# Kernel optimization log

Measured on AMD Instinct MI355X. Metric: run time of the kernel, lower is better.

Reference implementation:

```python
import jax, jax.numpy as jnp
import numpy as np

K = 1024            # atoms per chain
L = 4 * K - 9       # 2*(K-3) sin/cos dihedrals + (K-2) len13 + (K-1) bond lengths
EPS = 1e-6


def _denorm(v, lo, hi):
    # map [-1, 1] -> [lo, hi]
    return (v + 1.0) * 0.5 * (hi - lo) + lo


def _output_arr2values(v):
    # split flat NN output into (sin/cos dihedrals, hedron len13, bond lengths)
    n_d = K - 3
    sc = v[: 2 * n_d].reshape(n_d, 2)                     # (sin, cos) per dihedral
    d13 = _denorm(v[2 * n_d : 2 * n_d + K - 2], 1.5, 5.0)  # 1-3 distances, [1.5, 5]
    bl = _denorm(v[2 * n_d + K - 2 :], 0.9, 3.0)           # bond lengths,  [0.9, 3]
    return sc, d13, bl


def _len2ang(sc, d13, bl):
    # bond angles via law of cosines from consecutive bond lengths + 1-3 distance
    l1, l2 = bl[:-1], bl[1:]
    ct = (l1 * l1 + l2 * l2 - d13 * d13) / (2.0 * l1 * l2)
    theta = jnp.arccos(jnp.clip(ct, -1.0 + EPS, 1.0 - EPS))   # (K-2,) radians
    chi = jnp.arctan2(sc[:, 0], sc[:, 1])                      # (K-3,) radians
    return theta, chi


def _len_ang2coords(bl, theta, chi):
    # sequential NeRF chain extension: place atom i from atoms i-3, i-2, i-1
    a0 = jnp.zeros(3, dtype=bl.dtype)
    a1 = jnp.array([1.0, 0.0, 0.0], dtype=bl.dtype) * bl[0]
    t0 = theta[0]
    a2 = a1 + bl[1] * jnp.stack([-jnp.cos(t0), jnp.sin(t0), jnp.zeros((), bl.dtype)])

    def step(carry, inp):
        a, b, c = carry
        l, th, ch = inp
        bc = c - b
        bc = bc / (jnp.linalg.norm(bc) + EPS)
        n = jnp.cross(b - a, bc)
        n = n / (jnp.linalg.norm(n) + EPS)
        m = jnp.cross(n, bc)
        st = jnp.sin(th)
        d = c + l * (-jnp.cos(th) * bc + st * jnp.cos(ch) * m + st * jnp.sin(ch) * n)
        return (b, c, d), d

    _, rest = jax.lax.scan(step, (a0, a1, a2), (bl[2:], theta[1:], chi))
    return jnp.concatenate([jnp.stack([a0, a1, a2]), rest], axis=0)  # (K, 3)


def _chain2coords(v):
    sc, d13, bl = _output_arr2values(v)
    theta, chi = _len2ang(sc, d13, bl)
    return _len_ang2coords(bl, theta, chi)


def setup_inputs() -> dict:
    key = jax.random.key(0)
    k1, k2 = jax.random.split(key)
    B = 2048
    predictions = 2.0 * jax.random.uniform(k1, (B, L), dtype=jnp.float32) - 1.0
    targets = 2.0 * jax.random.uniform(k2, (B, L), dtype=jnp.float32) - 1.0
    return {"predictions": predictions, "targets": targets}


def reference(predictions, targets):
    p = jnp.clip(predictions, -1.0, 1.0)           # only predictions are clamped
    pred_coords = jax.vmap(_chain2coords)(p)        # (B, K, 3)
    targ_coords = jax.vmap(_chain2coords)(targets)  # (B, K, 3)
    return jnp.mean(jnp.square(pred_coords - targ_coords))
```

## Files before the change

### kernel.cpp

```cpp
#include <hip/hip_runtime.h>


#define LROW  4087
#define NSTEP 1021
#define NROW  2048
#define CHUNK 8
#define EPSF  1e-6f
#define INVMEAN (1.0f / (2048.0f * 1024.0f * 3.0f))

__device__ __forceinline__ float frcp(float x){ return __builtin_amdgcn_rcpf(x); }
__device__ __forceinline__ float frsq(float x){ return __builtin_amdgcn_rsqf(x); }

struct Xf { float f[12]; };

__device__ __forceinline__ Xf xident(){
  Xf X;
  X.f[0]=1.f; X.f[1]=0.f; X.f[2]=0.f;
  X.f[3]=0.f; X.f[4]=1.f; X.f[5]=0.f;
  X.f[6]=0.f; X.f[7]=0.f; X.f[8]=1.f;
  X.f[9]=0.f; X.f[10]=0.f; X.f[11]=0.f;
  return X;
}

__device__ __forceinline__ Xf xcombine(const Xf& A, const Xf& B){
  Xf C;
  #pragma unroll
  for (int c3 = 0; c3 < 12; c3 += 3){
    const float bx = B.f[c3], by = B.f[c3+1], bz = B.f[c3+2];
    C.f[c3]   = A.f[0]*bx + A.f[3]*by + A.f[6]*bz;
    C.f[c3+1] = A.f[1]*bx + A.f[4]*by + A.f[7]*bz;
    C.f[c3+2] = A.f[2]*bx + A.f[5]*by + A.f[8]*bz;
  }
  C.f[9] += A.f[9]; C.f[10] += A.f[10]; C.f[11] += A.f[11];
  return C;
}

__device__ __forceinline__ void xstepP(Xf& X, float Px, float Py, float Pz){
  const float l2 = Px*Px + Py*Py + Pz*Pz;
  const float q  = frsq(l2);
  const float hx = q*Px, hy = q*Py, hz = q*Pz;
  const float ist = frsq(fmaxf(hy*hy + hz*hz, 1e-12f));
  const float ux = X.f[0]*Px + X.f[3]*Py + X.f[6]*Pz;
  const float uy = X.f[1]*Px + X.f[4]*Py + X.f[7]*Pz;
  const float uz = X.f[2]*Px + X.f[5]*Py + X.f[8]*Pz;
  X.f[9] += ux; X.f[10] += uy; X.f[11] += uz;
  const float n0x = q*ux, n0y = q*uy, n0z = q*uz;
  const float n1x = ist*(hx*n0x - X.f[0]);
  const float n1y = ist*(hx*n0y - X.f[1]);
  const float n1z = ist*(hx*n0z - X.f[2]);
  const float n2x = ist*(hy*X.f[6] - hz*X.f[3]);
  const float n2y = ist*(hy*X.f[7] - hz*X.f[4]);
  const float n2z = ist*(hy*X.f[8] - hz*X.f[5]);
  X.f[0]=n0x; X.f[1]=n0y; X.f[2]=n0z;
  X.f[3]=n1x; X.f[4]=n1y; X.f[5]=n1z;
  X.f[6]=n2x; X.f[7]=n2y; X.f[8]=n2z;
}

__device__ __forceinline__ void xinitP(Xf& X, float Px, float Py, float Pz){
  const float l2 = Px*Px + Py*Py + Pz*Pz;
  const float q  = frsq(l2);
  const float hx = q*Px, hy = q*Py, hz = q*Pz;
  const float s2 = fmaxf(hy*hy + hz*hz, 1e-12f);
  const float ist = frsq(s2);
  const float st  = s2 * ist;
  X.f[0]=hx;        X.f[1]=hy;          X.f[2]=hz;
  X.f[3]=-st;       X.f[4]=hx*hy*ist;   X.f[5]=hx*hz*ist;
  X.f[6]=0.f;       X.f[7]=-hz*ist;     X.f[8]=hy*ist;
  X.f[9]=Px;        X.f[10]=Py;         X.f[11]=Pz;
}

__global__ void __launch_bounds__(256, 4)
rmsd_kernel(const float* __restrict__ pred, const float* __restrict__ targ,
            float* __restrict__ out){
  __shared__ float pos[128*25 + 8];
  __shared__ float Tbuf[2][12];
  __shared__ float ini[3];
  __shared__ float part;

  const int row  = blockIdx.x;
  const int tid  = threadIdx.x;
  const int ln   = tid & 63;
  const int wv   = tid >> 6;
  const int c    = wv >> 1;
  const int half = wv & 1;
  const int lid  = (half << 6) | ln;
  const int j0   = lid * CHUNK;

  const float* __restrict__ v = (c ? targ : pred) + (size_t)row * LROW;
  const float cl = c ? 1e30f : 1.0f;

  const float rb0 = fminf(fmaxf(v[3064], -cl), cl);
  const float rd0 = fminf(fmaxf(v[2042], -cl), cl);
  const float rb1 = fminf(fmaxf(v[3065], -cl), cl);

  float s0[CHUNK], s1[CHUNK], dd[CHUNK], bv[CHUNK+1];
  #pragma unroll
  for (int k = 0; k < CHUNK; ++k){
    s0[k] = v[2*(j0+k)];
    s1[k] = v[2*(j0+k)+1];
    dd[k] = v[2043 + j0 + k];
  }
  #pragma unroll
  for (int m = 0; m <= CHUNK; ++m){
    int ix = 3065 + j0 + m;
    if (ix > 4086) ix = 4086;
    bv[m] = v[ix];
  }

  #pragma unroll
  for (int m = 0; m <= CHUNK; ++m)
    bv[m] = fmaf(fminf(fmaxf(bv[m], -cl), cl), 1.05f, 1.95f);

  float Px[CHUNK], Py[CHUNK], Pz[CHUNK];
  #pragma unroll
  for (int k = 0; k < CHUNK; ++k){
    const float a0 = fminf(fmaxf(s0[k], -cl), cl);
    const float a1 = fminf(fmaxf(s1[k], -cl), cl);
    const float d  = fmaf(fminf(fmaxf(dd[k], -cl), cl), 1.75f, 3.25f);
    const float b1 = bv[k], b2 = bv[k+1];
    float ct = (b1*b1 + b2*b2 - d*d) * frcp(2.0f*b1*b2);
    ct = fminf(fmaxf(ct, -1.0f + EPSF), 1.0f - EPSF);
    const float st = sqrtf(fmaxf(1.0f - ct*ct, 0.0f));
    const float r2 = a0*a0 + a1*a1;
    const bool ok = r2 > 1e-36f;
    const float ir = ok ? frcp(sqrtf(r2)) : 0.0f;
    const float scv = a0 * ir;
    const float ccv = ok ? a1 * ir : 1.0f;
    Px[k] = -b2 * ct;
    Py[k] = b2 * st * ccv;
    Pz[k] = b2 * st * scv;
  }

  Xf X;
  float tl[CHUNK][3];
  xinitP(X, Px[0], Py[0], Pz[0]);
  tl[0][0]=X.f[9]; tl[0][1]=X.f[10]; tl[0][2]=X.f[11];
  #pragma unroll
  for (int k = 1; k < CHUNK; ++k){
    if (j0 + k < NSTEP) xstepP(X, Px[k], Py[k], Pz[k]);
    tl[k][0]=X.f[9]; tl[k][1]=X.f[10]; tl[k][2]=X.f[11];
  }

  #pragma unroll
  for (int off = 1; off < 64; off <<= 1){
    Xf o;
    #pragma unroll
    for (int i = 0; i < 12; ++i) o.f[i] = __shfl_up(X.f[i], off);
    if (ln >= off) X = xcombine(o, X);
  }

  if (half == 0 && ln == 63){
    #pragma unroll
    for (int i = 0; i < 12; ++i) Tbuf[c][i] = X.f[i];
  }

  Xf E;
  #pragma unroll
  for (int i = 0; i < 12; ++i) E.f[i] = __shfl_up(X.f[i], 1);
  if (ln == 0) E = xident();

  __syncthreads();

  if (half == 1){
    Xf T;
    #pragma unroll
    for (int i = 0; i < 12; ++i) T.f[i] = Tbuf[c][i];
    E = xcombine(T, E);
  }

  const float bl0 = fmaf(rb0, 1.05f, 1.95f);
  const float d0  = fmaf(rd0, 1.75f, 3.25f);
  const float b1f = fmaf(rb1, 1.05f, 1.95f);
  float ct0 = (bl0*bl0 + b1f*b1f - d0*d0) * frcp(2.0f*bl0*b1f);
  ct0 = fminf(fmaxf(ct0, -1.0f + EPSF), 1.0f - EPSF);
  const float st0 = sqrtf(fmaxf(1.0f - ct0*ct0, 0.0f));
  const float a1x = bl0;
  const float a2x = bl0 - b1f*ct0;
  const float a2y = b1f*st0;

  Xf G;
  #pragma unroll
  for (int c3 = 0; c3 < 12; c3 += 3){
    const float ex = E.f[c3], ey = E.f[c3+1], ez = E.f[c3+2];
    G.f[c3]   = -ct0*ex - st0*ey;
    G.f[c3+1] =  st0*ex - ct0*ey;
    G.f[c3+2] =  ez;
  }
  G.f[9] += a2x; G.f[10] += a2y;

  #pragma unroll
  for (int k = 0; k < CHUNK; ++k){
    const float tx = tl[k][0], ty = tl[k][1], tz = tl[k][2];
    tl[k][0] = G.f[9]  + G.f[0]*tx + G.f[3]*ty + G.f[6]*tz;
    tl[k][1] = G.f[10] + G.f[1]*tx + G.f[4]*ty + G.f[7]*tz;
    tl[k][2] = G.f[11] + G.f[2]*tx + G.f[5]*ty + G.f[8]*tz;
  }

  if (c == 0){
    #pragma unroll
    for (int k = 0; k < CHUNK; ++k){
      if (j0 + k < NSTEP){
        const int o = lid*25 + 3*k;
        pos[o] = tl[k][0]; pos[o+1] = tl[k][1]; pos[o+2] = tl[k][2];
      }
    }
    if (lid == 0){ ini[0] = a1x; ini[1] = a2x; ini[2] = a2y; }
  }
  __syncthreads();

  float acc = 0.0f;
  if (c == 1){
    if (lid == 0){
      const float dx = ini[0] - a1x;
      const float dy = ini[1] - a2x;
      const float dz = ini[2] - a2y;
      acc = dx*dx + dy*dy + dz*dz;
    }
    #pragma unroll
    for (int k = 0; k < CHUNK; ++k){
      if (j0 + k < NSTEP){
        const int o = lid*25 + 3*k;
        const float dx = pos[o]   - tl[k][0];
        const float dy = pos[o+1] - tl[k][1];
        const float dz = pos[o+2] - tl[k][2];
        acc = fmaf(dx, dx, acc);
        acc = fmaf(dy, dy, acc);
        acc = fmaf(dz, dz, acc);
      }
    }
    #pragma unroll
    for (int off = 32; off > 0; off >>= 1) acc += __shfl_down(acc, off);
    if (half == 1 && ln == 0) part = acc;
  }
  __syncthreads();
  if (wv == 2 && ln == 0) atomicAdd(out, (acc + part) * INVMEAN);
}

extern "C" void kernel_launch(void* const* d_in, const int* in_sizes, int n_in,
                              void* d_out, int out_size, void* d_ws, size_t ws_size,
                              hipStream_t stream) {
  const float* pred = (const float*)d_in[0];
  const float* targ = (const float*)d_in[1];
  float* out = (float*)d_out;

  hipMemsetAsync(d_out, 0, sizeof(float), stream);
  rmsd_kernel<<<NROW, 256, 0, stream>>>(pred, targ, out);
}
```

Measured before the change: 118.9 us.

## Represent chain frames as quaternions and scan rotations and translations separately

Each NeRF step's frame update is now a unit quaternion built from half-angle sines and cosines, instead of a 3x4 affine matrix updated with rsqrt normalisation. The cross-lane prefix scan combines 4-float quaternions rather than 12-float affine transforms. Translations are rotated by the exclusive quaternion prefix and summed with a separate 3-float additive scan. The goal is fewer shuffles and less arithmetic per scan level and lower register pressure. The trade-off is extra sqrt calls per step and different numerical behaviour, including unnormalised quaternion drift and the tail handling for j0+k>=NSTEP, which is no longer guarded inside the chunk.

New measurement: 138.4 us. 1.16x slower.

```diff
diff --git a/kernel.cpp b/kernel.cpp
--- a/kernel.cpp
+++ b/kernel.cpp
@@ -9,71 +9,33 @@
 #define INVMEAN (1.0f / (2048.0f * 1024.0f * 3.0f))
 
 __device__ __forceinline__ float frcp(float x){ return __builtin_amdgcn_rcpf(x); }
-__device__ __forceinline__ float frsq(float x){ return __builtin_amdgcn_rsqf(x); }
-
-struct Xf { float f[12]; };
-
-__device__ __forceinline__ Xf xident(){
-  Xf X;
-  X.f[0]=1.f; X.f[1]=0.f; X.f[2]=0.f;
-  X.f[3]=0.f; X.f[4]=1.f; X.f[5]=0.f;
-  X.f[6]=0.f; X.f[7]=0.f; X.f[8]=1.f;
-  X.f[9]=0.f; X.f[10]=0.f; X.f[11]=0.f;
-  return X;
-}
-
-__device__ __forceinline__ Xf xcombine(const Xf& A, const Xf& B){
-  Xf C;
-  #pragma unroll
-  for (int c3 = 0; c3 < 12; c3 += 3){
-    const float bx = B.f[c3], by = B.f[c3+1], bz = B.f[c3+2];
-    C.f[c3]   = A.f[0]*bx + A.f[3]*by + A.f[6]*bz;
-    C.f[c3+1] = A.f[1]*bx + A.f[4]*by + A.f[7]*bz;
-    C.f[c3+2] = A.f[2]*bx + A.f[5]*by + A.f[8]*bz;
-  }
-  C.f[9] += A.f[9]; C.f[10] += A.f[10]; C.f[11] += A.f[11];
-  return C;
-}
-
-__device__ __forceinline__ void xstepP(Xf& X, float Px, float Py, float Pz){
-  const float l2 = Px*Px + Py*Py + Pz*Pz;
-  const float q  = frsq(l2);
-  const float hx = q*Px, hy = q*Py, hz = q*Pz;
-  const float ist = frsq(fmaxf(hy*hy + hz*hz, 1e-12f));
-  const float ux = X.f[0]*Px + X.f[3]*Py + X.f[6]*Pz;
-  const float uy = X.f[1]*Px + X.f[4]*Py + X.f[7]*Pz;
-  const float uz = X.f[2]*Px + X.f[5]*Py + X.f[8]*Pz;
-  X.f[9] += ux; X.f[10] += uy; X.f[11] += uz;
-  const float n0x = q*ux, n0y = q*uy, n0z = q*uz;
-  const float n1x = ist*(hx*n0x - X.f[0]);
-  const float n1y = ist*(hx*n0y - X.f[1]);
-  const float n1z = ist*(hx*n0z - X.f[2]);
-  const float n2x = ist*(hy*X.f[6] - hz*X.f[3]);
-  const float n2y = ist*(hy*X.f[7] - hz*X.f[4]);
-  const float n2z = ist*(hy*X.f[8] - hz*X.f[5]);
-  X.f[0]=n0x; X.f[1]=n0y; X.f[2]=n0z;
-  X.f[3]=n1x; X.f[4]=n1y; X.f[5]=n1z;
-  X.f[6]=n2x; X.f[7]=n2y; X.f[8]=n2z;
-}
-
-__device__ __forceinline__ void xinitP(Xf& X, float Px, float Py, float Pz){
-  const float l2 = Px*Px + Py*Py + Pz*Pz;
-  const float q  = frsq(l2);
-  const float hx = q*Px, hy = q*Py, hz = q*Pz;
-  const float s2 = fmaxf(hy*hy + hz*hz, 1e-12f);
-  const float ist = frsq(s2);
-  const float st  = s2 * ist;
-  X.f[0]=hx;        X.f[1]=hy;          X.f[2]=hz;
-  X.f[3]=-st;       X.f[4]=hx*hy*ist;   X.f[5]=hx*hz*ist;
-  X.f[6]=0.f;       X.f[7]=-hz*ist;     X.f[8]=hy*ist;
-  X.f[9]=Px;        X.f[10]=Py;         X.f[11]=Pz;
+
+struct Q { float w, x, y, z; };
+
+__device__ __forceinline__ Q qmul(const Q a, const Q b){
+  Q c;
+  c.w = a.w*b.w - a.x*b.x - a.y*b.y - a.z*b.z;
+  c.x = a.w*b.x + a.x*b.w + a.y*b.z - a.z*b.y;
+  c.y = a.w*b.y - a.x*b.z + a.y*b.w + a.z*b.x;
+  c.z = a.w*b.z + a.x*b.y - a.y*b.x + a.z*b.w;
+  return c;
+}
+
+__device__ __forceinline__ void qrot(const Q q, float vx, float vy, float vz,
+                                     float& rx, float& ry, float& rz){
+  const float cx = q.y*vz - q.z*vy + q.w*vx;
+  const float cy = q.z*vx - q.x*vz + q.w*vy;
+  const float cz = q.x*vy - q.y*vx + q.w*vz;
+  rx = fmaf(2.f, q.y*cz - q.z*cy, vx);
+  ry = fmaf(2.f, q.z*cx - q.x*cz, vy);
+  rz = fmaf(2.f, q.x*cy - q.y*cx, vz);
 }
 
 __global__ void __launch_bounds__(256, 4)
 rmsd_kernel(const float* __restrict__ pred, const float* __restrict__ targ,
             float* __restrict__ out){
   __shared__ float pos[128*25 + 8];
-  __shared__ float Tbuf[2][12];
+  __shared__ float Tbuf[2][8];
   __shared__ float ini[3];
   __shared__ float part;
 
@@ -106,12 +68,12 @@
     if (ix > 4086) ix = 4086;
     bv[m] = v[ix];
   }
-
   #pragma unroll
   for (int m = 0; m <= CHUNK; ++m)
     bv[m] = fmaf(fminf(fmaxf(bv[m], -cl), cl), 1.05f, 1.95f);
 
-  float Px[CHUNK], Py[CHUNK], Pz[CHUNK];
+  float tlx[CHUNK], tly[CHUNK], tlz[CHUNK];
+  Q q;
   #pragma unroll
   for (int k = 0; k < CHUNK; ++k){
     const float a0 = fminf(fmaxf(s0[k], -cl), cl);
@@ -126,46 +88,65 @@
     const float ir = ok ? frcp(sqrtf(r2)) : 0.0f;
     const float scv = a0 * ir;
     const float ccv = ok ? a1 * ir : 1.0f;
-    Px[k] = -b2 * ct;
-    Py[k] = b2 * st * ccv;
-    Pz[k] = b2 * st * scv;
-  }
-
-  Xf X;
-  float tl[CHUNK][3];
-  xinitP(X, Px[0], Py[0], Pz[0]);
-  tl[0][0]=X.f[9]; tl[0][1]=X.f[10]; tl[0][2]=X.f[11];
-  #pragma unroll
-  for (int k = 1; k < CHUNK; ++k){
-    if (j0 + k < NSTEP) xstepP(X, Px[k], Py[k], Pz[k]);
-    tl[k][0]=X.f[9]; tl[k][1]=X.f[10]; tl[k][2]=X.f[11];
+    const float bst = b2 * st;
+    const float Px = -b2*ct, Py = bst*ccv, Pz = bst*scv;
+    const float ca2 = sqrtf(0.5f*(1.0f - ct));
+    const float sa2 = sqrtf(0.5f*(1.0f + ct));
+    const float cb2 = sqrtf(fmaxf(0.5f*(1.0f + ccv), 0.0f));
+    const float sb2 = __builtin_copysignf(
+                        sqrtf(fmaxf(0.5f*(1.0f - ccv), 0.0f)), scv);
+    Q qs; qs.w = cb2*ca2; qs.x = sb2*ca2; qs.y = -sb2*sa2; qs.z = cb2*sa2;
+    if (k == 0){
+      tlx[0] = Px; tly[0] = Py; tlz[0] = Pz;
+      q = qs;
+    } else {
+      float rx, ry, rz;
+      qrot(q, Px, Py, Pz, rx, ry, rz);
+      tlx[k] = tlx[k-1] + rx; tly[k] = tly[k-1] + ry; tlz[k] = tlz[k-1] + rz;
+      q = qmul(q, qs);
+    }
   }
 
   #pragma unroll
   for (int off = 1; off < 64; off <<= 1){
-    Xf o;
-    #pragma unroll
-    for (int i = 0; i < 12; ++i) o.f[i] = __shfl_up(X.f[i], off);
-    if (ln >= off) X = xcombine(o, X);
-  }
+    Q o;
+    o.w = __shfl_up(q.w, off); o.x = __shfl_up(q.x, off);
+    o.y = __shfl_up(q.y, off); o.z = __shfl_up(q.z, off);
+    const bool pr = (ln >= off);
+    o.w = pr ? o.w : 1.0f; o.x = pr ? o.x : 0.0f;
+    o.y = pr ? o.y : 0.0f; o.z = pr ? o.z : 0.0f;
+    q = qmul(o, q);
+  }
+
+  Q qe;
+  qe.w = __shfl_up(q.w, 1); qe.x = __shfl_up(q.x, 1);
+  qe.y = __shfl_up(q.y, 1); qe.z = __shfl_up(q.z, 1);
+  if (ln == 0){ qe.w = 1.0f; qe.x = 0.0f; qe.y = 0.0f; qe.z = 0.0f; }
+
+  float wx, wy, wz;
+  qrot(qe, tlx[CHUNK-1], tly[CHUNK-1], tlz[CHUNK-1], wx, wy, wz);
+  float sx = wx, sy = wy, sz = wz;
+  #pragma unroll
+  for (int off = 1; off < 64; off <<= 1){
+    const float ax = __shfl_up(sx, off);
+    const float ay = __shfl_up(sy, off);
+    const float az = __shfl_up(sz, off);
+    if (ln >= off){ sx += ax; sy += ay; sz += az; }
+  }
+  float tex = sx - wx, tey = sy - wy, tez = sz - wz;
 
   if (half == 0 && ln == 63){
-    #pragma unroll
-    for (int i = 0; i < 12; ++i) Tbuf[c][i] = X.f[i];
-  }
-
-  Xf E;
-  #pragma unroll
-  for (int i = 0; i < 12; ++i) E.f[i] = __shfl_up(X.f[i], 1);
-  if (ln == 0) E = xident();
-
+    Tbuf[c][0] = q.w; Tbuf[c][1] = q.x; Tbuf[c][2] = q.y; Tbuf[c][3] = q.z;
+    Tbuf[c][4] = sx;  Tbuf[c][5] = sy;  Tbuf[c][6] = sz;
+  }
   __syncthreads();
 
   if (half == 1){
-    Xf T;
-    #pragma unroll
-    for (int i = 0; i < 12; ++i) T.f[i] = Tbuf[c][i];
-    E = xcombine(T, E);
+    Q T; T.w = Tbuf[c][0]; T.x = Tbuf[c][1]; T.y = Tbuf[c][2]; T.z = Tbuf[c][3];
+    float rx, ry, rz;
+    qrot(T, tex, tey, tez, rx, ry, rz);
+    tex = Tbuf[c][4] + rx; tey = Tbuf[c][5] + ry; tez = Tbuf[c][6] + rz;
+    qe = qmul(T, qe);
   }
 
   const float bl0 = fmaf(rb0, 1.05f, 1.95f);
@@ -178,22 +159,34 @@
   const float a2x = bl0 - b1f*ct0;
   const float a2y = b1f*st0;
 
-  Xf G;
-  #pragma unroll
-  for (int c3 = 0; c3 < 12; c3 += 3){
-    const float ex = E.f[c3], ey = E.f[c3+1], ez = E.f[c3+2];
-    G.f[c3]   = -ct0*ex - st0*ey;
-    G.f[c3+1] =  st0*ex - ct0*ey;
-    G.f[c3+2] =  ez;
-  }
-  G.f[9] += a2x; G.f[10] += a2y;
+  const float cg2 = sqrtf(0.5f*(1.0f - ct0));
+  const float sg2 = sqrtf(0.5f*(1.0f + ct0));
+  Q g;
+  g.w = cg2*qe.w - sg2*qe.z;
+  g.x = cg2*qe.x - sg2*qe.y;
+  g.y = cg2*qe.y + sg2*qe.x;
+  g.z = cg2*qe.z + sg2*qe.w;
+
+  const float gtx = a2x + (-ct0*tex - st0*tey);
+  const float gty = a2y + ( st0*tex - ct0*tey);
+  const float gtz = tez;
+
+  const float nrm = g.w*g.w + g.x*g.x + g.y*g.y + g.z*g.z;
+  const float s2n = 2.0f * frcp(nrm);
+  const float xs = g.x*s2n, ys = g.y*s2n, zs = g.z*s2n;
+  const float wxm = g.w*xs, wym = g.w*ys, wzm = g.w*zs;
+  const float xxm = g.x*xs, xym = g.x*ys, xzm = g.x*zs;
+  const float yym = g.y*ys, yzm = g.y*zs, zzm = g.z*zs;
+  const float m00 = 1.0f-(yym+zzm), m01 = xym-wzm,        m02 = xzm+wym;
+  const float m10 = xym+wzm,        m11 = 1.0f-(xxm+zzm), m12 = yzm-wxm;
+  const float m20 = xzm-wym,        m21 = yzm+wxm,        m22 = 1.0f-(xxm+yym);
 
   #pragma unroll
   for (int k = 0; k < CHUNK; ++k){
-    const float tx = tl[k][0], ty = tl[k][1], tz = tl[k][2];
-    tl[k][0] = G.f[9]  + G.f[0]*tx + G.f[3]*ty + G.f[6]*tz;
-    tl[k][1] = G.f[10] + G.f[1]*tx + G.f[4]*ty + G.f[7]*tz;
-    tl[k][2] = G.f[11] + G.f[2]*tx + G.f[5]*ty + G.f[8]*tz;
+    const float tx = tlx[k], ty = tly[k], tz = tlz[k];
+    tlx[k] = gtx + m00*tx + m01*ty + m02*tz;
+    tly[k] = gty + m10*tx + m11*ty + m12*tz;
+    tlz[k] = gtz + m20*tx + m21*ty + m22*tz;
   }
 
   if (c == 0){
@@ -201,7 +194,7 @@
     for (int k = 0; k < CHUNK; ++k){
       if (j0 + k < NSTEP){
         const int o = lid*25 + 3*k;
-        pos[o] = tl[k][0]; pos[o+1] = tl[k][1]; pos[o+2] = tl[k][2];
+        pos[o] = tlx[k]; pos[o+1] = tly[k]; pos[o+2] = tlz[k];
       }
     }
     if (lid == 0){ ini[0] = a1x; ini[1] = a2x; ini[2] = a2y; }
@@ -220,9 +213,9 @@
     for (int k = 0; k < CHUNK; ++k){
       if (j0 + k < NSTEP){
         const int o = lid*25 + 3*k;
-        const float dx = pos[o]   - tl[k][0];
-        const float dy = pos[o+1] - tl[k][1];
-        const float dz = pos[o+2] - tl[k][2];
+        const float dx = pos[o]   - tlx[k];
+        const float dy = pos[o+1] - tly[k];
+        const float dz = pos[o+2] - tlz[k];
         acc = fmaf(dx, dx, acc);
         acc = fmaf(dy, dy, acc);
         acc = fmaf(dz, dz, acc);
```
